# Kernel optimization log

Measured on AMD Instinct MI355X. Metric: run time of the kernel, lower is better.

Reference implementation:

```python
import jax, jax.numpy as jnp
import numpy as np

CHANNELS = 8
IN_CHANNELS = 8
MASK_OUT_STRIDE = 4
WEIGHT_NUMS = [(IN_CHANNELS + 2) * CHANNELS, CHANNELS * CHANNELS, CHANNELS * 1]
BIAS_NUMS = [CHANNELS, CHANNELS, 1]
SOI = jnp.array([8.0, 16.0, 32.0, 64.0, 128.0], dtype=jnp.float32)
EPS = 1e-5


def compute_locations(h, w, stride):
    # (x, y) center of each stride-sized cell, row-major (y outer, x inner)
    sx = jnp.arange(w, dtype=jnp.float32) * stride + stride // 2
    sy = jnp.arange(h, dtype=jnp.float32) * stride + stride // 2
    yy, xx = jnp.meshgrid(sy, sx, indexing='ij')
    return jnp.stack([xx.reshape(-1), yy.reshape(-1)], axis=-1)  # [H*W, 2]


def aligned_bilinear(t, factor):
    # Matches AdelaiDet aligned_bilinear: replicate-pad right/bottom, bilinear
    # upsample align_corners=True to (f*h+1, f*w+1), replicate-pad top/left by
    # f//2, crop to (f*h, f*w).
    if factor == 1:
        return t
    n, c, h, w = t.shape
    t = jnp.pad(t, ((0, 0), (0, 0), (0, 1), (0, 1)), mode='edge')  # [n,c,h+1,w+1]
    oh, ow = factor * h + 1, factor * w + 1
    ys = jnp.arange(oh, dtype=jnp.float32) / factor  # align_corners mapping
    xs = jnp.arange(ow, dtype=jnp.float32) / factor
    y0 = jnp.floor(ys).astype(jnp.int32)
    x0 = jnp.floor(xs).astype(jnp.int32)
    y1 = jnp.minimum(y0 + 1, h)
    x1 = jnp.minimum(x0 + 1, w)
    wy = (ys - y0.astype(jnp.float32)).astype(t.dtype)
    wx = (xs - x0.astype(jnp.float32)).astype(t.dtype)
    ty = t[:, :, y0, :] * (1.0 - wy)[None, None, :, None] + t[:, :, y1, :] * wy[None, None, :, None]
    out = ty[:, :, :, x0] * (1.0 - wx) + ty[:, :, :, x1] * wx
    p = factor // 2
    out = jnp.pad(out, ((0, 0), (0, 0), (p, 0), (p, 0)), mode='edge')
    return out[:, :, :oh - 1, :ow - 1]


def parse_dynamic_params(params):
    n = params.shape[0]
    splits = jnp.split(params, np.cumsum(WEIGHT_NUMS + BIAS_NUMS)[:-1], axis=1)
    w0 = splits[0].reshape(n, CHANNELS, IN_CHANNELS + 2)
    w1 = splits[1].reshape(n, CHANNELS, CHANNELS)
    w2 = splits[2].reshape(n, 1, CHANNELS)
    b0 = splits[3].reshape(n, CHANNELS)
    b1 = splits[4].reshape(n, CHANNELS)
    b2 = splits[5].reshape(n, 1)
    return (w0, w1, w2), (b0, b1, b2)


def setup_inputs() -> dict:
    key = jax.random.key(0)
    ks = jax.random.split(key, 6)
    N, H, W = 2, 100, 136
    n_inst = 500
    return {
        'mask_feats': jax.random.normal(ks[0], (N, IN_CHANNELS, H, W), dtype=jnp.float32),
        'mask_head_params': jax.random.normal(ks[1], (n_inst, 169), dtype=jnp.float32),
        'locations_inst': jax.random.uniform(ks[2], (n_inst, 2), dtype=jnp.float32),
        'gt_bitmasks': jax.random.uniform(ks[3], (n_inst, 1, 2 * H, 2 * W), dtype=jnp.float32),
        'im_inds': jax.random.randint(ks[4], (n_inst,), 0, N, dtype=jnp.int64 if jax.config.jax_enable_x64 else jnp.int32),
        'fpn_levels': jax.random.randint(ks[5], (n_inst,), 0, 5, dtype=jnp.int64 if jax.config.jax_enable_x64 else jnp.int32),
        'mask_feat_stride': 8,
    }


def reference(mask_feats, mask_head_params, locations_inst, gt_bitmasks, im_inds, fpn_levels, mask_feat_stride):
    N, Cin, H, W = mask_feats.shape
    n = mask_head_params.shape[0]
    # relative coordinates, normalized by per-instance size-of-interest
    locs = compute_locations(H, W, mask_feat_stride)                 # [HW, 2]
    rel = locations_inst[:, None, :] - locs[None, :, :]              # [n, HW, 2]
    rel = jnp.transpose(rel, (0, 2, 1))                              # [n, 2, HW]
    soi = SOI[fpn_levels]                                            # [n]
    rel = (rel / soi[:, None, None]).astype(mask_feats.dtype)
    feats = mask_feats[im_inds].reshape(n, Cin, H * W)               # gather per instance
    x = jnp.concatenate([rel, feats], axis=1)                        # [n, Cin+2, HW]
    # per-instance 1x1 conv stack == batched small GEMMs
    (w0, w1, w2), (b0, b1, b2) = parse_dynamic_params(mask_head_params)
    x = jax.nn.relu(jnp.einsum('nci,nip->ncp', w0, x) + b0[:, :, None])
    x = jax.nn.relu(jnp.einsum('nci,nip->ncp', w1, x) + b1[:, :, None])
    x = jnp.einsum('nci,nip->ncp', w2, x) + b2[:, :, None]           # [n, 1, HW]
    logits = x.reshape(n, 1, H, W)
    logits = aligned_bilinear(logits, mask_feat_stride // MASK_OUT_STRIDE)
    scores = jax.nn.sigmoid(logits)                                  # [n, 1, 2H, 2W]
    # dice loss
    xs = scores.reshape(n, -1)
    t = gt_bitmasks.reshape(n, -1)
    inter = jnp.sum(xs * t, axis=1)
    union = jnp.sum(xs * xs, axis=1) + jnp.sum(t * t, axis=1) + EPS
    loss = 1.0 - 2.0 * inter / union
    return jnp.mean(loss)
```

## Files before the change

kernel.cpp:

```cpp
#include <hip/hip_runtime.h>
#include <hip/hip_bf16.h>
#include <math.h>

#define CIN      8
#define H_IN     100
#define W_IN     136
#define NPIX     (H_IN * W_IN)
#define OH       (2 * H_IN)
#define OW       (2 * W_IN)
#define ONPIX    (OH * OW)
#define NPARAMS  169
#define EPSV     1e-5f
#define NSLICE   4
#define KG4      34
#define KGROUPS  34
#define TASKS_B  (25 * KGROUPS)


__device__ __forceinline__ float sigmoidf_fast(float x) {
    float e = __expf(-x);
    return __builtin_amdgcn_rcpf(1.f + e);
}

__global__ __launch_bounds__(256, 2)
void mask_head_fused(const float* __restrict__ mask_feats,
                     const float* __restrict__ params,
                     const float* __restrict__ locs,
                     const float* __restrict__ gt,
                     const int*   __restrict__ im_inds,
                     const int*   __restrict__ fpn_levels,
                     float*       __restrict__ partials)
{
    const int inst  = blockIdx.x >> 2;
    const int slice = blockIdx.x & 3;
    const int tid   = threadIdx.x;

    const int r_start = (slice == 0) ? 0 : 25 * slice - 1;
    const int nrows   = (slice == 0) ? 25 : 26;
    const int ntask   = nrows * KG4;

    __shared__ float s_logit[26 * W_IN];
    __shared__ float s_red[12];

    const float* __restrict__ wp = params + (size_t)inst * NPARAMS;

    const int   im  = im_inds[inst];
    const int   lvl = fpn_levels[inst];
    const float inv_soi = exp2f(-(float)(3 + lvl));
    const float lx = locs[inst * 2 + 0];
    const float ly = locs[inst * 2 + 1];
    const float dx8 = 8.f * inv_soi;

    const float* feat = mask_feats + (size_t)im * (CIN * NPIX);
    const int goff = r_start * W_IN;

    #pragma unroll 1
    for (int it = 0; it < 4; ++it) {
        const int t = it * 256 + tid;
        const bool valid = t < ntask;
        const int tc = valid ? t : ntask - 1;
        const int r  = tc / KG4;
        const int k  = tc - r * KG4;
        const int lpx = r * W_IN + 4 * k;
        const float* fb = feat + (goff + lpx);

        float4 f0 = *(const float4*)(fb);
        float4 f1 = *(const float4*)(fb + NPIX);
        float4 f2 = *(const float4*)(fb + 2 * NPIX);
        float4 f3 = *(const float4*)(fb + 3 * NPIX);
        float4 f4 = *(const float4*)(fb + 4 * NPIX);
        float4 f5 = *(const float4*)(fb + 5 * NPIX);
        float4 f6 = *(const float4*)(fb + 6 * NPIX);
        float4 f7 = *(const float4*)(fb + 7 * NPIX);

        float in0[4];
        in0[0] = (lx - (float)(32 * k + 4)) * inv_soi;
        in0[1] = in0[0] - dx8;
        in0[2] = in0[1] - dx8;
        in0[3] = in0[2] - dx8;
        const float in1 = (ly - (float)((r_start + r) * 8 + 4)) * inv_soi;

        float a[8][4];
        #pragma unroll
        for (int o = 0; o < 8; ++o) {
            const float b  = wp[152 + o];
            const float w0 = wp[o * 10 + 0];
            const float w1 = wp[o * 10 + 1];
            const float base = fmaf(w1, in1, b);
            #pragma unroll
            for (int j = 0; j < 4; ++j)
                a[o][j] = fmaf(w0, in0[j], base);
        }
        const float* fc[8][1];
        float f[8][4];
        f[0][0]=f0.x; f[0][1]=f0.y; f[0][2]=f0.z; f[0][3]=f0.w;
        f[1][0]=f1.x; f[1][1]=f1.y; f[1][2]=f1.z; f[1][3]=f1.w;
        f[2][0]=f2.x; f[2][1]=f2.y; f[2][2]=f2.z; f[2][3]=f2.w;
        f[3][0]=f3.x; f[3][1]=f3.y; f[3][2]=f3.z; f[3][3]=f3.w;
        f[4][0]=f4.x; f[4][1]=f4.y; f[4][2]=f4.z; f[4][3]=f4.w;
        f[5][0]=f5.x; f[5][1]=f5.y; f[5][2]=f5.z; f[5][3]=f5.w;
        f[6][0]=f6.x; f[6][1]=f6.y; f[6][2]=f6.z; f[6][3]=f6.w;
        f[7][0]=f7.x; f[7][1]=f7.y; f[7][2]=f7.z; f[7][3]=f7.w;
        (void)fc;
        #pragma unroll
        for (int c = 0; c < CIN; ++c) {
            #pragma unroll
            for (int o = 0; o < 8; ++o) {
                const float w = wp[o * 10 + 2 + c];
                a[o][0] = fmaf(w, f[c][0], a[o][0]);
                a[o][1] = fmaf(w, f[c][1], a[o][1]);
                a[o][2] = fmaf(w, f[c][2], a[o][2]);
                a[o][3] = fmaf(w, f[c][3], a[o][3]);
            }
        }
        #pragma unroll
        for (int o = 0; o < 8; ++o) {
            a[o][0] = fmaxf(a[o][0], 0.f);
            a[o][1] = fmaxf(a[o][1], 0.f);
            a[o][2] = fmaxf(a[o][2], 0.f);
            a[o][3] = fmaxf(a[o][3], 0.f);
        }

        float h[8][4];
        #pragma unroll
        for (int o = 0; o < 8; ++o) {
            const float b = wp[160 + o];
            h[o][0] = b; h[o][1] = b; h[o][2] = b; h[o][3] = b;
        }
        #pragma unroll
        for (int i = 0; i < 8; ++i) {
            #pragma unroll
            for (int o = 0; o < 8; ++o) {
                const float w = wp[80 + o * 8 + i];
                h[o][0] = fmaf(w, a[i][0], h[o][0]);
                h[o][1] = fmaf(w, a[i][1], h[o][1]);
                h[o][2] = fmaf(w, a[i][2], h[o][2]);
                h[o][3] = fmaf(w, a[i][3], h[o][3]);
            }
        }

        const float b2 = wp[168];
        float o4[4] = {b2, b2, b2, b2};
        #pragma unroll
        for (int i = 0; i < 8; ++i) {
            const float w = wp[144 + i];
            o4[0] = fmaf(w, fmaxf(h[i][0], 0.f), o4[0]);
            o4[1] = fmaf(w, fmaxf(h[i][1], 0.f), o4[1]);
            o4[2] = fmaf(w, fmaxf(h[i][2], 0.f), o4[2]);
            o4[3] = fmaf(w, fmaxf(h[i][3], 0.f), o4[3]);
        }

        if (valid) {
            float4 ov = {o4[0], o4[1], o4[2], o4[3]};
            *(float4*)(s_logit + lpx) = ov;
        }
    }

    __syncthreads();

    float inter = 0.f, ssum = 0.f, tsum = 0.f;
    const float* gtp = gt + (size_t)inst * ONPIX;
    const int pair_base = 25 * slice;

    #pragma unroll 1
    for (int base = 0; base < TASKS_B; base += 256) {
        const int task = base + tid;
        if (task < TASKS_B) {
            const int pl = task / KGROUPS;
            const int k  = task - pl * KGROUPS;
            const int pg = pair_base + pl;
            const int er = pg - r_start;
            const int pr = (pg > 0 ? pg - 1 : 0) - r_start;
            const float* E = s_logit + er * W_IN;
            const float* P = s_logit + pr * W_IN;
            const int c0  = 4 * k;
            const int cm1 = (k > 0) ? c0 - 1 : 0;

            const float4 e4 = *(const float4*)(E + c0);
            const float  em = E[cm1];
            const float4 p4 = *(const float4*)(P + c0);
            const float  pm = P[cm1];

            const float* g0 = gtp + (size_t)(2 * pg) * OW + 8 * k;
            const float4 ga = *(const float4*)(g0);
            const float4 gb = *(const float4*)(g0 + 4);
            const float4 gc = *(const float4*)(g0 + OW);
            const float4 gd = *(const float4*)(g0 + OW + 4);

            const float ecur[4] = {e4.x, e4.y, e4.z, e4.w};
            const float pcur[4] = {p4.x, p4.y, p4.z, p4.w};
            const float gav[8]  = {ga.x, ga.y, ga.z, ga.w, gb.x, gb.y, gb.z, gb.w};
            const float gex[8]  = {gc.x, gc.y, gc.z, gc.w, gd.x, gd.y, gd.z, gd.w};

            float Se_prev = em;
            float Sa_prev = 0.5f * (em + pm);
            #pragma unroll
            for (int j = 0; j < 4; ++j) {
                const float Se = ecur[j];
                const float Sa = 0.5f * (ecur[j] + pcur[j]);
                {
                    float s = sigmoidf_fast(0.5f * (Sa_prev + Sa));
                    float t = gav[2 * j];
                    inter = fmaf(s, t, inter); ssum = fmaf(s, s, ssum); tsum = fmaf(t, t, tsum);
                    s = sigmoidf_fast(Sa);
                    t = gav[2 * j + 1];
                    inter = fmaf(s, t, inter); ssum = fmaf(s, s, ssum); tsum = fmaf(t, t, tsum);
                }
                {
                    float s = sigmoidf_fast(0.5f * (Se_prev + Se));
                    float t = gex[2 * j];
                    inter = fmaf(s, t, inter); ssum = fmaf(s, s, ssum); tsum = fmaf(t, t, tsum);
                    s = sigmoidf_fast(Se);
                    t = gex[2 * j + 1];
                    inter = fmaf(s, t, inter); ssum = fmaf(s, s, ssum); tsum = fmaf(t, t, tsum);
                }
                Se_prev = Se;
                Sa_prev = Sa;
            }
        }
    }

    #pragma unroll
    for (int off = 32; off > 0; off >>= 1) {
        inter += __shfl_down(inter, off, 64);
        ssum  += __shfl_down(ssum,  off, 64);
        tsum  += __shfl_down(tsum,  off, 64);
    }
    const int wid = tid >> 6;
    if ((tid & 63) == 0) {
        s_red[wid * 3 + 0] = inter;
        s_red[wid * 3 + 1] = ssum;
        s_red[wid * 3 + 2] = tsum;
    }
    __syncthreads();
    if (tid == 0) {
        float I = 0.f, S = 0.f, T = 0.f;
        #pragma unroll
        for (int w = 0; w < 4; ++w) {
            I += s_red[w * 3 + 0];
            S += s_red[w * 3 + 1];
            T += s_red[w * 3 + 2];
        }
        partials[blockIdx.x * 3 + 0] = I;
        partials[blockIdx.x * 3 + 1] = S;
        partials[blockIdx.x * 3 + 2] = T;
    }
}

__global__ __launch_bounds__(512)
void loss_mean_kernel(const float* __restrict__ partials, float* __restrict__ out, int n)
{
    __shared__ float s_red[8];
    float v = 0.f;
    for (int i = threadIdx.x; i < n; i += 512) {
        float I = 0.f, S = 0.f, T = 0.f;
        #pragma unroll
        for (int s = 0; s < NSLICE; ++s) {
            const float* p = partials + (size_t)(i * NSLICE + s) * 3;
            I += p[0];
            S += p[1];
            T += p[2];
        }
        v += 1.f - 2.f * I / (S + T + EPSV);
    }
    #pragma unroll
    for (int off = 32; off > 0; off >>= 1) v += __shfl_down(v, off, 64);
    const int wid = threadIdx.x >> 6;
    if ((threadIdx.x & 63) == 0) s_red[wid] = v;
    __syncthreads();
    if (threadIdx.x == 0) {
        float s = 0.f;
        #pragma unroll
        for (int w = 0; w < 8; ++w) s += s_red[w];
        out[0] = s / (float)n;
    }
}

extern "C" void kernel_launch(void* const* d_in, const int* in_sizes, int n_in,
                              void* d_out, int out_size, void* d_ws, size_t ws_size,
                              hipStream_t stream)
{
    const float* mask_feats = (const float*)d_in[0];
    const float* params     = (const float*)d_in[1];
    const float* locs       = (const float*)d_in[2];
    const float* gt         = (const float*)d_in[3];
    const int*   im_inds    = (const int*)d_in[4];
    const int*   fpn_levels = (const int*)d_in[5];

    const int n = in_sizes[4];
    float* partials = (float*)d_ws;

    mask_head_fused<<<n * NSLICE, 256, 0, stream>>>(mask_feats, params, locs, gt,
                                                    im_inds, fpn_levels, partials);
    loss_mean_kernel<<<1, 512, 0, stream>>>(partials, (float*)d_out, n);
}
```

Before: 182.8 us.

## Software-pipeline feature and mask loads with double-buffered registers across both phases

The kernel's fixed four-iteration loops in the conv phase and the dice phase become explicit unrolled sequences. Global loads for the next task are issued before the current task is computed, using two or three register buffers. The ground-truth loads for the dice phase are also issued before the barrier that separates the phases, so they overlap with waiting on the other waves. The intent is to hide global memory latency, at the cost of higher register pressure that may lower occupancy under the existing launch bounds.

```diff
diff --git a/kernel.cpp b/kernel.cpp
--- a/kernel.cpp
+++ b/kernel.cpp
@@ -54,24 +54,21 @@
     const float* feat = mask_feats + (size_t)im * (CIN * NPIX);
     const int goff = r_start * W_IN;
 
-    #pragma unroll 1
-    for (int it = 0; it < 4; ++it) {
-        const int t = it * 256 + tid;
+    auto loadA = [&](float4* f, int t) {
+        const int tc = t < ntask ? t : ntask - 1;
+        const int r  = tc / KG4;
+        const int k  = tc - r * KG4;
+        const float* fb = feat + (goff + r * W_IN + 4 * k);
+        #pragma unroll
+        for (int c = 0; c < CIN; ++c)
+            f[c] = *(const float4*)(fb + c * NPIX);
+    };
+    auto computeA = [&](const float4* f, int t) {
         const bool valid = t < ntask;
         const int tc = valid ? t : ntask - 1;
         const int r  = tc / KG4;
         const int k  = tc - r * KG4;
         const int lpx = r * W_IN + 4 * k;
-        const float* fb = feat + (goff + lpx);
-
-        float4 f0 = *(const float4*)(fb);
-        float4 f1 = *(const float4*)(fb + NPIX);
-        float4 f2 = *(const float4*)(fb + 2 * NPIX);
-        float4 f3 = *(const float4*)(fb + 3 * NPIX);
-        float4 f4 = *(const float4*)(fb + 4 * NPIX);
-        float4 f5 = *(const float4*)(fb + 5 * NPIX);
-        float4 f6 = *(const float4*)(fb + 6 * NPIX);
-        float4 f7 = *(const float4*)(fb + 7 * NPIX);
 
         float in0[4];
         in0[0] = (lx - (float)(32 * k + 4)) * inv_soi;
@@ -83,59 +80,45 @@
         float a[8][4];
         #pragma unroll
         for (int o = 0; o < 8; ++o) {
-            const float b  = wp[152 + o];
+            const float base = fmaf(wp[o * 10 + 1], in1, wp[152 + o]);
             const float w0 = wp[o * 10 + 0];
-            const float w1 = wp[o * 10 + 1];
-            const float base = fmaf(w1, in1, b);
             #pragma unroll
             for (int j = 0; j < 4; ++j)
                 a[o][j] = fmaf(w0, in0[j], base);
         }
-        const float* fc[8][1];
-        float f[8][4];
-        f[0][0]=f0.x; f[0][1]=f0.y; f[0][2]=f0.z; f[0][3]=f0.w;
-        f[1][0]=f1.x; f[1][1]=f1.y; f[1][2]=f1.z; f[1][3]=f1.w;
-        f[2][0]=f2.x; f[2][1]=f2.y; f[2][2]=f2.z; f[2][3]=f2.w;
-        f[3][0]=f3.x; f[3][1]=f3.y; f[3][2]=f3.z; f[3][3]=f3.w;
-        f[4][0]=f4.x; f[4][1]=f4.y; f[4][2]=f4.z; f[4][3]=f4.w;
-        f[5][0]=f5.x; f[5][1]=f5.y; f[5][2]=f5.z; f[5][3]=f5.w;
-        f[6][0]=f6.x; f[6][1]=f6.y; f[6][2]=f6.z; f[6][3]=f6.w;
-        f[7][0]=f7.x; f[7][1]=f7.y; f[7][2]=f7.z; f[7][3]=f7.w;
-        (void)fc;
         #pragma unroll
         for (int c = 0; c < CIN; ++c) {
+            const float4 fc = f[c];
+            const float fv[4] = {fc.x, fc.y, fc.z, fc.w};
             #pragma unroll
             for (int o = 0; o < 8; ++o) {
                 const float w = wp[o * 10 + 2 + c];
-                a[o][0] = fmaf(w, f[c][0], a[o][0]);
-                a[o][1] = fmaf(w, f[c][1], a[o][1]);
-                a[o][2] = fmaf(w, f[c][2], a[o][2]);
-                a[o][3] = fmaf(w, f[c][3], a[o][3]);
+                #pragma unroll
+                for (int j = 0; j < 4; ++j)
+                    a[o][j] = fmaf(w, fv[j], a[o][j]);
             }
         }
         #pragma unroll
-        for (int o = 0; o < 8; ++o) {
-            a[o][0] = fmaxf(a[o][0], 0.f);
-            a[o][1] = fmaxf(a[o][1], 0.f);
-            a[o][2] = fmaxf(a[o][2], 0.f);
-            a[o][3] = fmaxf(a[o][3], 0.f);
-        }
+        for (int o = 0; o < 8; ++o)
+            #pragma unroll
+            for (int j = 0; j < 4; ++j)
+                a[o][j] = fmaxf(a[o][j], 0.f);
 
         float h[8][4];
         #pragma unroll
         for (int o = 0; o < 8; ++o) {
             const float b = wp[160 + o];
-            h[o][0] = b; h[o][1] = b; h[o][2] = b; h[o][3] = b;
+            #pragma unroll
+            for (int j = 0; j < 4; ++j) h[o][j] = b;
         }
         #pragma unroll
         for (int i = 0; i < 8; ++i) {
             #pragma unroll
             for (int o = 0; o < 8; ++o) {
                 const float w = wp[80 + o * 8 + i];
-                h[o][0] = fmaf(w, a[i][0], h[o][0]);
-                h[o][1] = fmaf(w, a[i][1], h[o][1]);
-                h[o][2] = fmaf(w, a[i][2], h[o][2]);
-                h[o][3] = fmaf(w, a[i][3], h[o][3]);
+                #pragma unroll
+                for (int j = 0; j < 4; ++j)
+                    h[o][j] = fmaf(w, a[i][j], h[o][j]);
             }
         }
 
@@ -144,80 +127,105 @@
         #pragma unroll
         for (int i = 0; i < 8; ++i) {
             const float w = wp[144 + i];
-            o4[0] = fmaf(w, fmaxf(h[i][0], 0.f), o4[0]);
-            o4[1] = fmaf(w, fmaxf(h[i][1], 0.f), o4[1]);
-            o4[2] = fmaf(w, fmaxf(h[i][2], 0.f), o4[2]);
-            o4[3] = fmaf(w, fmaxf(h[i][3], 0.f), o4[3]);
+            #pragma unroll
+            for (int j = 0; j < 4; ++j)
+                o4[j] = fmaf(w, fmaxf(h[i][j], 0.f), o4[j]);
         }
 
         if (valid) {
             float4 ov = {o4[0], o4[1], o4[2], o4[3]};
             *(float4*)(s_logit + lpx) = ov;
         }
-    }
-
-    __syncthreads();
+    };
+
+    {
+        float4 fA[8], fB[8];
+        const int t0 = tid, t1 = tid + 256, t2 = tid + 512, t3 = tid + 768;
+        loadA(fA, t0);
+        loadA(fB, t1);
+        computeA(fA, t0);
+        loadA(fA, t2);
+        computeA(fB, t1);
+        loadA(fB, t3);
+        computeA(fA, t2);
+        computeA(fB, t3);
+    }
 
     float inter = 0.f, ssum = 0.f, tsum = 0.f;
     const float* gtp = gt + (size_t)inst * ONPIX;
     const int pair_base = 25 * slice;
 
-    #pragma unroll 1
-    for (int base = 0; base < TASKS_B; base += 256) {
-        const int task = base + tid;
-        if (task < TASKS_B) {
-            const int pl = task / KGROUPS;
-            const int k  = task - pl * KGROUPS;
-            const int pg = pair_base + pl;
-            const int er = pg - r_start;
-            const int pr = (pg > 0 ? pg - 1 : 0) - r_start;
-            const float* E = s_logit + er * W_IN;
-            const float* P = s_logit + pr * W_IN;
-            const int c0  = 4 * k;
-            const int cm1 = (k > 0) ? c0 - 1 : 0;
-
-            const float4 e4 = *(const float4*)(E + c0);
-            const float  em = E[cm1];
-            const float4 p4 = *(const float4*)(P + c0);
-            const float  pm = P[cm1];
-
-            const float* g0 = gtp + (size_t)(2 * pg) * OW + 8 * k;
-            const float4 ga = *(const float4*)(g0);
-            const float4 gb = *(const float4*)(g0 + 4);
-            const float4 gc = *(const float4*)(g0 + OW);
-            const float4 gd = *(const float4*)(g0 + OW + 4);
-
-            const float ecur[4] = {e4.x, e4.y, e4.z, e4.w};
-            const float pcur[4] = {p4.x, p4.y, p4.z, p4.w};
-            const float gav[8]  = {ga.x, ga.y, ga.z, ga.w, gb.x, gb.y, gb.z, gb.w};
-            const float gex[8]  = {gc.x, gc.y, gc.z, gc.w, gd.x, gd.y, gd.z, gd.w};
-
-            float Se_prev = em;
-            float Sa_prev = 0.5f * (em + pm);
-            #pragma unroll
-            for (int j = 0; j < 4; ++j) {
-                const float Se = ecur[j];
-                const float Sa = 0.5f * (ecur[j] + pcur[j]);
-                {
-                    float s = sigmoidf_fast(0.5f * (Sa_prev + Sa));
-                    float t = gav[2 * j];
-                    inter = fmaf(s, t, inter); ssum = fmaf(s, s, ssum); tsum = fmaf(t, t, tsum);
-                    s = sigmoidf_fast(Sa);
-                    t = gav[2 * j + 1];
-                    inter = fmaf(s, t, inter); ssum = fmaf(s, s, ssum); tsum = fmaf(t, t, tsum);
-                }
-                {
-                    float s = sigmoidf_fast(0.5f * (Se_prev + Se));
-                    float t = gex[2 * j];
-                    inter = fmaf(s, t, inter); ssum = fmaf(s, s, ssum); tsum = fmaf(t, t, tsum);
-                    s = sigmoidf_fast(Se);
-                    t = gex[2 * j + 1];
-                    inter = fmaf(s, t, inter); ssum = fmaf(s, s, ssum); tsum = fmaf(t, t, tsum);
-                }
-                Se_prev = Se;
-                Sa_prev = Sa;
+    auto loadB = [&](float4* g, int t) {
+        const int tc = t < TASKS_B ? t : TASKS_B - 1;
+        const int pl = tc / KGROUPS;
+        const int k  = tc - pl * KGROUPS;
+        const float* g0 = gtp + (size_t)(2 * (pair_base + pl)) * OW + 8 * k;
+        g[0] = *(const float4*)(g0);
+        g[1] = *(const float4*)(g0 + 4);
+        g[2] = *(const float4*)(g0 + OW);
+        g[3] = *(const float4*)(g0 + OW + 4);
+    };
+    auto computeB = [&](const float4* g, int t) {
+        if (t >= TASKS_B) return;
+        const int pl = t / KGROUPS;
+        const int k  = t - pl * KGROUPS;
+        const int pg = pair_base + pl;
+        const int er = pg - r_start;
+        const int pr = (pg > 0 ? pg - 1 : 0) - r_start;
+        const float* E = s_logit + er * W_IN;
+        const float* P = s_logit + pr * W_IN;
+        const int c0  = 4 * k;
+        const int cm1 = (k > 0) ? c0 - 1 : 0;
+
+        const float4 e4 = *(const float4*)(E + c0);
+        const float  em = E[cm1];
+        const float4 p4 = *(const float4*)(P + c0);
+        const float  pm = P[cm1];
+
+        const float ecur[4] = {e4.x, e4.y, e4.z, e4.w};
+        const float pcur[4] = {p4.x, p4.y, p4.z, p4.w};
+        const float gav[8] = {g[0].x, g[0].y, g[0].z, g[0].w, g[1].x, g[1].y, g[1].z, g[1].w};
+        const float gex[8] = {g[2].x, g[2].y, g[2].z, g[2].w, g[3].x, g[3].y, g[3].z, g[3].w};
+
+        float Se_prev = em;
+        float Sa_prev = 0.5f * (em + pm);
+        #pragma unroll
+        for (int j = 0; j < 4; ++j) {
+            const float Se = ecur[j];
+            const float Sa = 0.5f * (ecur[j] + pcur[j]);
+            {
+                float s = sigmoidf_fast(0.5f * (Sa_prev + Sa));
+                float t2 = gav[2 * j];
+                inter = fmaf(s, t2, inter); ssum = fmaf(s, s, ssum); tsum = fmaf(t2, t2, tsum);
+                s = sigmoidf_fast(Sa);
+                t2 = gav[2 * j + 1];
+                inter = fmaf(s, t2, inter); ssum = fmaf(s, s, ssum); tsum = fmaf(t2, t2, tsum);
             }
-        }
+            {
+                float s = sigmoidf_fast(0.5f * (Se_prev + Se));
+                float t2 = gex[2 * j];
+                inter = fmaf(s, t2, inter); ssum = fmaf(s, s, ssum); tsum = fmaf(t2, t2, tsum);
+                s = sigmoidf_fast(Se);
+                t2 = gex[2 * j + 1];
+                inter = fmaf(s, t2, inter); ssum = fmaf(s, s, ssum); tsum = fmaf(t2, t2, tsum);
+            }
+            Se_prev = Se;
+            Sa_prev = Sa;
+        }
+    };
+
+    {
+        float4 ga[4], gb[4], gc[4];
+        const int t0 = tid, t1 = tid + 256, t2 = tid + 512, t3 = tid + 768;
+        loadB(ga, t0);
+        loadB(gb, t1);
+        __syncthreads();
+        loadB(gc, t2);
+        computeB(ga, t0);
+        loadB(ga, t3);
+        computeB(gb, t1);
+        computeB(gc, t2);
+        computeB(ga, t3);
     }
 
     #pragma unroll
```

Measured after the change: 185.0 us. About the same (+1.2%).

## Split fused mask head into separate logits and dice-reduce kernels via global buffer

Applied to the files above, without the earlier changes.

Splits the fused kernel in two. The first computes per-instance logits and writes them to a global workspace buffer. The second reads those logits and the ground truth to compute the upsampled sigmoid dice partials. This removes the halo-row recomputation and the shared-memory staging, and lets each kernel have its own occupancy (the dice kernel uses launch bounds of 3). In exchange it adds a global round trip for the logits (about 500*13600 floats, roughly 27 MB written and read) plus an extra kernel launch.

```diff
diff --git a/kernel.cpp b/kernel.cpp
--- a/kernel.cpp
+++ b/kernel.cpp
@@ -14,6 +14,7 @@
 #define NSLICE   4
 #define KG4      34
 #define KGROUPS  34
+#define TASKS_A  (25 * KG4)
 #define TASKS_B  (25 * KGROUPS)
 
 
@@ -23,24 +24,17 @@
 }
 
 __global__ __launch_bounds__(256, 2)
-void mask_head_fused(const float* __restrict__ mask_feats,
-                     const float* __restrict__ params,
-                     const float* __restrict__ locs,
-                     const float* __restrict__ gt,
-                     const int*   __restrict__ im_inds,
-                     const int*   __restrict__ fpn_levels,
-                     float*       __restrict__ partials)
+void mask_logits(const float* __restrict__ mask_feats,
+                 const float* __restrict__ params,
+                 const float* __restrict__ locs,
+                 const int*   __restrict__ im_inds,
+                 const int*   __restrict__ fpn_levels,
+                 float*       __restrict__ logits)
 {
     const int inst  = blockIdx.x >> 2;
     const int slice = blockIdx.x & 3;
     const int tid   = threadIdx.x;
-
-    const int r_start = (slice == 0) ? 0 : 25 * slice - 1;
-    const int nrows   = (slice == 0) ? 25 : 26;
-    const int ntask   = nrows * KG4;
-
-    __shared__ float s_logit[26 * W_IN];
-    __shared__ float s_red[12];
+    const int row0  = 25 * slice;
 
     const float* __restrict__ wp = params + (size_t)inst * NPARAMS;
 
@@ -52,17 +46,17 @@
     const float dx8 = 8.f * inv_soi;
 
     const float* feat = mask_feats + (size_t)im * (CIN * NPIX);
-    const int goff = r_start * W_IN;
+    float* lg = logits + (size_t)inst * NPIX;
 
     #pragma unroll 1
     for (int it = 0; it < 4; ++it) {
         const int t = it * 256 + tid;
-        const bool valid = t < ntask;
-        const int tc = valid ? t : ntask - 1;
-        const int r  = tc / KG4;
-        const int k  = tc - r * KG4;
-        const int lpx = r * W_IN + 4 * k;
-        const float* fb = feat + (goff + lpx);
+        if (t >= TASKS_A) break;
+        const int r  = t / KG4;
+        const int k  = t - r * KG4;
+        const int row = row0 + r;
+        const int px  = row * W_IN + 4 * k;
+        const float* fb = feat + px;
 
         float4 f0 = *(const float4*)(fb);
         float4 f1 = *(const float4*)(fb + NPIX);
@@ -78,20 +72,17 @@
         in0[1] = in0[0] - dx8;
         in0[2] = in0[1] - dx8;
         in0[3] = in0[2] - dx8;
-        const float in1 = (ly - (float)((r_start + r) * 8 + 4)) * inv_soi;
+        const float in1 = (ly - (float)(row * 8 + 4)) * inv_soi;
 
         float a[8][4];
         #pragma unroll
         for (int o = 0; o < 8; ++o) {
-            const float b  = wp[152 + o];
+            const float base = fmaf(wp[o * 10 + 1], in1, wp[152 + o]);
             const float w0 = wp[o * 10 + 0];
-            const float w1 = wp[o * 10 + 1];
-            const float base = fmaf(w1, in1, b);
             #pragma unroll
             for (int j = 0; j < 4; ++j)
                 a[o][j] = fmaf(w0, in0[j], base);
         }
-        const float* fc[8][1];
         float f[8][4];
         f[0][0]=f0.x; f[0][1]=f0.y; f[0][2]=f0.z; f[0][3]=f0.w;
         f[1][0]=f1.x; f[1][1]=f1.y; f[1][2]=f1.z; f[1][3]=f1.w;
@@ -101,41 +92,37 @@
         f[5][0]=f5.x; f[5][1]=f5.y; f[5][2]=f5.z; f[5][3]=f5.w;
         f[6][0]=f6.x; f[6][1]=f6.y; f[6][2]=f6.z; f[6][3]=f6.w;
         f[7][0]=f7.x; f[7][1]=f7.y; f[7][2]=f7.z; f[7][3]=f7.w;
-        (void)fc;
         #pragma unroll
         for (int c = 0; c < CIN; ++c) {
             #pragma unroll
             for (int o = 0; o < 8; ++o) {
                 const float w = wp[o * 10 + 2 + c];
-                a[o][0] = fmaf(w, f[c][0], a[o][0]);
-                a[o][1] = fmaf(w, f[c][1], a[o][1]);
-                a[o][2] = fmaf(w, f[c][2], a[o][2]);
-                a[o][3] = fmaf(w, f[c][3], a[o][3]);
-            }
-        }
-        #pragma unroll
-        for (int o = 0; o < 8; ++o) {
-            a[o][0] = fmaxf(a[o][0], 0.f);
-            a[o][1] = fmaxf(a[o][1], 0.f);
-            a[o][2] = fmaxf(a[o][2], 0.f);
-            a[o][3] = fmaxf(a[o][3], 0.f);
-        }
+                #pragma unroll
+                for (int j = 0; j < 4; ++j)
+                    a[o][j] = fmaf(w, f[c][j], a[o][j]);
+            }
+        }
+        #pragma unroll
+        for (int o = 0; o < 8; ++o)
+            #pragma unroll
+            for (int j = 0; j < 4; ++j)
+                a[o][j] = fmaxf(a[o][j], 0.f);
 
         float h[8][4];
         #pragma unroll
         for (int o = 0; o < 8; ++o) {
             const float b = wp[160 + o];
-            h[o][0] = b; h[o][1] = b; h[o][2] = b; h[o][3] = b;
+            #pragma unroll
+            for (int j = 0; j < 4; ++j) h[o][j] = b;
         }
         #pragma unroll
         for (int i = 0; i < 8; ++i) {
             #pragma unroll
             for (int o = 0; o < 8; ++o) {
                 const float w = wp[80 + o * 8 + i];
-                h[o][0] = fmaf(w, a[i][0], h[o][0]);
-                h[o][1] = fmaf(w, a[i][1], h[o][1]);
-                h[o][2] = fmaf(w, a[i][2], h[o][2]);
-                h[o][3] = fmaf(w, a[i][3], h[o][3]);
+                #pragma unroll
+                for (int j = 0; j < 4; ++j)
+                    h[o][j] = fmaf(w, a[i][j], h[o][j]);
             }
         }
 
@@ -144,79 +131,84 @@
         #pragma unroll
         for (int i = 0; i < 8; ++i) {
             const float w = wp[144 + i];
-            o4[0] = fmaf(w, fmaxf(h[i][0], 0.f), o4[0]);
-            o4[1] = fmaf(w, fmaxf(h[i][1], 0.f), o4[1]);
-            o4[2] = fmaf(w, fmaxf(h[i][2], 0.f), o4[2]);
-            o4[3] = fmaf(w, fmaxf(h[i][3], 0.f), o4[3]);
-        }
-
-        if (valid) {
-            float4 ov = {o4[0], o4[1], o4[2], o4[3]};
-            *(float4*)(s_logit + lpx) = ov;
-        }
-    }
-
-    __syncthreads();
+            #pragma unroll
+            for (int j = 0; j < 4; ++j)
+                o4[j] = fmaf(w, fmaxf(h[i][j], 0.f), o4[j]);
+        }
+
+        float4 ov = {o4[0], o4[1], o4[2], o4[3]};
+        *(float4*)(lg + px) = ov;
+    }
+}
+
+__global__ __launch_bounds__(256, 3)
+void dice_reduce(const float* __restrict__ logits,
+                 const float* __restrict__ gt,
+                 float*       __restrict__ partials)
+{
+    const int inst  = blockIdx.x >> 2;
+    const int slice = blockIdx.x & 3;
+    const int tid   = threadIdx.x;
+    const int pair_base = 25 * slice;
+
+    __shared__ float s_red[12];
+
+    const float* lg  = logits + (size_t)inst * NPIX;
+    const float* gtp = gt + (size_t)inst * ONPIX;
 
     float inter = 0.f, ssum = 0.f, tsum = 0.f;
-    const float* gtp = gt + (size_t)inst * ONPIX;
-    const int pair_base = 25 * slice;
 
     #pragma unroll 1
-    for (int base = 0; base < TASKS_B; base += 256) {
-        const int task = base + tid;
-        if (task < TASKS_B) {
-            const int pl = task / KGROUPS;
-            const int k  = task - pl * KGROUPS;
-            const int pg = pair_base + pl;
-            const int er = pg - r_start;
-            const int pr = (pg > 0 ? pg - 1 : 0) - r_start;
-            const float* E = s_logit + er * W_IN;
-            const float* P = s_logit + pr * W_IN;
-            const int c0  = 4 * k;
-            const int cm1 = (k > 0) ? c0 - 1 : 0;
-
-            const float4 e4 = *(const float4*)(E + c0);
-            const float  em = E[cm1];
-            const float4 p4 = *(const float4*)(P + c0);
-            const float  pm = P[cm1];
-
-            const float* g0 = gtp + (size_t)(2 * pg) * OW + 8 * k;
-            const float4 ga = *(const float4*)(g0);
-            const float4 gb = *(const float4*)(g0 + 4);
-            const float4 gc = *(const float4*)(g0 + OW);
-            const float4 gd = *(const float4*)(g0 + OW + 4);
-
-            const float ecur[4] = {e4.x, e4.y, e4.z, e4.w};
-            const float pcur[4] = {p4.x, p4.y, p4.z, p4.w};
-            const float gav[8]  = {ga.x, ga.y, ga.z, ga.w, gb.x, gb.y, gb.z, gb.w};
-            const float gex[8]  = {gc.x, gc.y, gc.z, gc.w, gd.x, gd.y, gd.z, gd.w};
-
-            float Se_prev = em;
-            float Sa_prev = 0.5f * (em + pm);
-            #pragma unroll
-            for (int j = 0; j < 4; ++j) {
-                const float Se = ecur[j];
-                const float Sa = 0.5f * (ecur[j] + pcur[j]);
-                {
-                    float s = sigmoidf_fast(0.5f * (Sa_prev + Sa));
-                    float t = gav[2 * j];
-                    inter = fmaf(s, t, inter); ssum = fmaf(s, s, ssum); tsum = fmaf(t, t, tsum);
-                    s = sigmoidf_fast(Sa);
-                    t = gav[2 * j + 1];
-                    inter = fmaf(s, t, inter); ssum = fmaf(s, s, ssum); tsum = fmaf(t, t, tsum);
-                }
-                {
-                    float s = sigmoidf_fast(0.5f * (Se_prev + Se));
-                    float t = gex[2 * j];
-                    inter = fmaf(s, t, inter); ssum = fmaf(s, s, ssum); tsum = fmaf(t, t, tsum);
-                    s = sigmoidf_fast(Se);
-                    t = gex[2 * j + 1];
-                    inter = fmaf(s, t, inter); ssum = fmaf(s, s, ssum); tsum = fmaf(t, t, tsum);
-                }
-                Se_prev = Se;
-                Sa_prev = Sa;
-            }
+    for (int it = 0; it < 4; ++it) {
+        const int t = it * 256 + tid;
+        if (t >= TASKS_B) break;
+        const int pl = t / KGROUPS;
+        const int k  = t - pl * KGROUPS;
+        const int pg = pair_base + pl;
+        const float* E = lg + pg * W_IN;
+        const float* P = lg + (pg > 0 ? pg - 1 : 0) * W_IN;
+        const int c0  = 4 * k;
+        const int cm1 = (k > 0) ? c0 - 1 : 0;
+
+        const float* g0 = gtp + (size_t)(2 * pg) * OW + 8 * k;
+        const float4 ga = *(const float4*)(g0);
+        const float4 gb = *(const float4*)(g0 + 4);
+        const float4 gc = *(const float4*)(g0 + OW);
+        const float4 gd = *(const float4*)(g0 + OW + 4);
+        const float4 e4 = *(const float4*)(E + c0);
+        const float  em = E[cm1];
+        const float4 p4 = *(const float4*)(P + c0);
+        const float  pm = P[cm1];
+
+        const float ecur[4] = {e4.x, e4.y, e4.z, e4.w};
+        const float pcur[4] = {p4.x, p4.y, p4.z, p4.w};
+        const float gav[8] = {ga.x, ga.y, ga.z, ga.w, gb.x, gb.y, gb.z, gb.w};
+        const float gex[8] = {gc.x, gc.y, gc.z, gc.w, gd.x, gd.y, gd.z, gd.w};
+
+        float Se_prev = em;
+        float Sa_prev = 0.5f * (em + pm);
+        #pragma unroll
+        for (int j = 0; j < 4; ++j) {
+            const float Se = ecur[j];
+            const float Sa = 0.5f * (ecur[j] + pcur[j]);
+            {
+                float s = sigmoidf_fast(0.5f * (Sa_prev + Sa));
+                float t2 = gav[2 * j];
+                inter = fmaf(s, t2, inter); ssum = fmaf(s, s, ssum); tsum = fmaf(t2, t2, tsum);
+                s = sigmoidf_fast(Sa);
+                t2 = gav[2 * j + 1];
+                inter = fmaf(s, t2, inter); ssum = fmaf(s, s, ssum); tsum = fmaf(t2, t2, tsum);
+            }
+            {
+                float s = sigmoidf_fast(0.5f * (Se_prev + Se));
+                float t2 = gex[2 * j];
+                inter = fmaf(s, t2, inter); ssum = fmaf(s, s, ssum); tsum = fmaf(t2, t2, tsum);
+                s = sigmoidf_fast(Se);
+                t2 = gex[2 * j + 1];
+                inter = fmaf(s, t2, inter); ssum = fmaf(s, s, ssum); tsum = fmaf(t2, t2, tsum);
+            }
+            Se_prev = Se;
+            Sa_prev = Sa;
         }
     }
 
@@ -288,9 +280,12 @@
     const int*   fpn_levels = (const int*)d_in[5];
 
     const int n = in_sizes[4];
-    float* partials = (float*)d_ws;
-
-    mask_head_fused<<<n * NSLICE, 256, 0, stream>>>(mask_feats, params, locs, gt,
-                                                    im_inds, fpn_levels, partials);
+
+    float* logits   = (float*)d_ws;
+    float* partials = logits + (size_t)n * NPIX;
+
+    mask_logits<<<n * NSLICE, 256, 0, stream>>>(mask_feats, params, locs,
+                                                im_inds, fpn_levels, logits);
+    dice_reduce<<<n * NSLICE, 256, 0, stream>>>(logits, gt, partials);
     loss_mean_kernel<<<1, 512, 0, stream>>>(partials, (float*)d_out, n);
 }
```

Result: slower. 213.8 us (+16.9%).
